# Performance work log

Measured on AMD Instinct MI355X. Metric: run time of the kernel, lower is better.

Reference implementation:

```python
import jax, jax.numpy as jnp
import numpy as np

D_MODEL = 1024
D_QK = 1024
NUM_HEADS = 16
HEAD_DIM = D_QK // NUM_HEADS      # 64
V_DIM = D_MODEL // NUM_HEADS      # 64
B, S = 2, 2048


def setup_inputs() -> dict:
    key = jax.random.key(0)
    ks = jax.random.split(key, 9)
    sc = 0.02
    return {
        "x": jax.random.normal(ks[0], (B, S, D_MODEL), dtype=jnp.float32),
        "Wqk": jax.random.normal(ks[1], (D_MODEL, 2 * D_QK), dtype=jnp.float32) * sc,
        "bqk": jax.random.normal(ks[2], (2 * D_QK,), dtype=jnp.float32) * sc,
        "Wv": jax.random.normal(ks[3], (D_MODEL, D_MODEL), dtype=jnp.float32) * sc,
        "bv": jax.random.normal(ks[4], (D_MODEL,), dtype=jnp.float32) * sc,
        "Wn": jax.random.normal(ks[5], (D_MODEL, NUM_HEADS), dtype=jnp.float32) * sc,
        "bn": jax.random.normal(ks[6], (NUM_HEADS,), dtype=jnp.float32) * sc,
        "Wo": jax.random.normal(ks[7], (D_MODEL, D_MODEL), dtype=jnp.float32) * sc,
        "bo": jax.random.normal(ks[8], (D_MODEL,), dtype=jnp.float32) * sc,
    }


def reference(x, Wqk, bqk, Wv, bv, Wn, bn, Wo, bo):
    b, s, _ = x.shape
    qk = x @ Wqk + bqk                                  # (B,S,2*D_QK)
    v = x @ Wv + bv                                     # (B,S,D_MODEL)
    n = x @ Wn + bn                                     # (B,S,H)

    qk = qk.reshape(b, s, 2, NUM_HEADS, HEAD_DIM)
    q, k = qk[:, :, 0], qk[:, :, 1]                     # (B,S,H,Dh)
    v = v.reshape(b, s, NUM_HEADS, V_DIM)               # (B,S,H,Dv)

    scores = jnp.einsum('bthd,bshd->bhts', q, k)        # (B,H,S,S)
    mask = jnp.tril(jnp.ones((s, s), dtype=scores.dtype))
    n_exp = jnp.exp(jnp.transpose(n, (0, 2, 1)))        # (B,H,S)
    attn = scores * mask / n_exp[:, :, :, None]         # dropout p=0 (eval)

    ctx = jnp.einsum('bhts,bshd->bthd', attn, v)        # (B,S,H,Dv)
    ctx = ctx.reshape(b, s, D_MODEL)
    return ctx @ Wo + bo
```

## Files before the change

### kernel.cpp

```cpp
#include <hip/hip_runtime.h>
#include <hip/hip_bf16.h>

constexpr int Bb   = 2;
constexpr int Ss   = 2048;
constexpr int Dm   = 1024;
constexpr int Hh   = 16;
constexpr int Hd   = 64;
constexpr int Mtot = Bb * Ss;
constexpr int NCH  = Ss / 64;

typedef __bf16 bf16x8 __attribute__((ext_vector_type(8)));
typedef float  f32x4  __attribute__((ext_vector_type(4)));
typedef __attribute__((address_space(1))) unsigned int u32_as1;
typedef __attribute__((address_space(3))) unsigned int u32_as3;

__device__ __forceinline__ void gload_lds16(const void* g, void* l) {
  __builtin_amdgcn_global_load_lds((const u32_as1*)g, (u32_as3*)l, 16, 0, 0);
}

__device__ __forceinline__ unsigned short f2bf(float f) {
  union { float f; unsigned u; } x; x.f = f;
  unsigned r = x.u + 0x7fffu + ((x.u >> 16) & 1u);
  return (unsigned short)(r >> 16);
}

__device__ __forceinline__ float bf2f(unsigned short s) {
  union { unsigned u; float f; } x; x.u = ((unsigned)s) << 16;
  return x.f;
}

__global__ __launch_bounds__(256) void k_prep(
    const float* __restrict__ x, const float* __restrict__ Wn, const float* __restrict__ bn,
    float* __restrict__ invn, unsigned short* __restrict__ xb,
    const float* __restrict__ Wqk, const float* __restrict__ Wv, const float* __restrict__ Wo,
    unsigned short* __restrict__ wprojT, unsigned short* __restrict__ woT) {
  __shared__ __align__(16) char smem[16384];
  int bi = blockIdx.x;
  int tid = threadIdx.x;
  if (bi < 1024) {
    float (*xl)[1024] = (float(*)[1024])smem;
    int w = tid >> 6, lane = tid & 63;
    int row = bi * 4 + w;
    const float4* x4 = (const float4*)(x + (size_t)row * Dm);
    ushort4* xb4 = (ushort4*)(xb + (size_t)row * Dm);
#pragma unroll
    for (int j = 0; j < 4; ++j) {
      float4 v = x4[j * 64 + lane];
      *(float4*)&xl[w][(j * 64 + lane) * 4] = v;
      ushort4 o;
      o.x = f2bf(v.x); o.y = f2bf(v.y); o.z = f2bf(v.z); o.w = f2bf(v.w);
      xb4[j * 64 + lane] = o;
    }
    __syncthreads();
    const float4* Wn4 = (const float4*)Wn;
    f32x4 sum = {0.f, 0.f, 0.f, 0.f};
#pragma unroll 4
    for (int j = 0; j < 64; ++j) {
      float xv = xl[w][j * 16 + (lane >> 2)];
      float4 wv = Wn4[j * 64 + lane];
      sum[0] += xv * wv.x; sum[1] += xv * wv.y; sum[2] += xv * wv.z; sum[3] += xv * wv.w;
    }
#pragma unroll
    for (int m = 4; m < 64; m <<= 1) {
      sum[0] += __shfl_xor(sum[0], m);
      sum[1] += __shfl_xor(sum[1], m);
      sum[2] += __shfl_xor(sum[2], m);
      sum[3] += __shfl_xor(sum[3], m);
    }
    if (lane < 4) {
      int b = row >> 11, s = row & 2047;
#pragma unroll
      for (int e = 0; e < 4; ++e) {
        int h = lane * 4 + e;
        float nv = sum[e] + bn[h];
        invn[((size_t)(b * Hh + h)) * Ss + s] = expf(-nv);
      }
    }
  } else {
    float (*t)[33] = (float(*)[33])smem;
    int ti = bi - 1024;
    const float* W; unsigned short* Wt; int N, n0, k0;
    if (ti < 2048) {
      W = Wqk; Wt = wprojT; N = 2048;
      n0 = (ti & 63) * 32; k0 = (ti >> 6) * 32;
    } else if (ti < 3072) {
      int l = ti - 2048; W = Wv; Wt = wprojT + (size_t)2048 * 1024; N = 1024;
      n0 = (l & 31) * 32; k0 = (l >> 5) * 32;
    } else {
      int l = ti - 3072; W = Wo; Wt = woT; N = 1024;
      n0 = (l & 31) * 32; k0 = (l >> 5) * 32;
    }
    int tx = tid & 31, ty = tid >> 5;
#pragma unroll
    for (int j = 0; j < 32; j += 8)
      t[ty + j][tx] = W[(size_t)(k0 + ty + j) * N + n0 + tx];
    __syncthreads();
#pragma unroll
    for (int j = 0; j < 32; j += 8)
      Wt[(size_t)(n0 + ty + j) * 1024 + k0 + tx] = f2bf(t[tx][ty + j]);
  }
}

__global__ __launch_bounds__(256, 4) void k_gemm_proj(
    const unsigned short* __restrict__ A, const unsigned short* __restrict__ BT,
    const float* __restrict__ bias0, const float* __restrict__ bias1,
    void* __restrict__ out0, void* __restrict__ out1, void* __restrict__ out2,
    void* __restrict__ out3, int M, int N, int K) {
  __shared__ __align__(16) unsigned short SMEM[2 * 128 * 64];
  unsigned short* As = SMEM;
  unsigned short* Bs = SMEM + 128 * 64;
  int tid = threadIdx.x, w = tid >> 6, lane = tid & 63;
  int bid = blockIdx.y * gridDim.x + blockIdx.x;
  int xcd = bid & 7, idx = bid >> 3;
  int m0 = (xcd * 4 + (idx & 3)) * 128;
  int n0 = (idx >> 2) * 128;
  int wm = w >> 1, wn = w & 1;
  f32x4 acc[4][4] = {};

  int csrc = 8 * ((lane & 7) ^ (lane >> 3));
  int rst  = w * 8 + (lane >> 3);
  int rxor = (lane & 7) << 3;

  for (int kt = 0; kt < (K >> 6); ++kt) {
#pragma unroll
    for (int i = 0; i < 4; ++i) {
      int r = i * 32 + rst;
      gload_lds16(A + (size_t)(m0 + r) * K + kt * 64 + csrc, As + i * 2048 + w * 512);
    }
#pragma unroll
    for (int i = 0; i < 4; ++i) {
      int r = i * 32 + rst;
      gload_lds16(BT + (size_t)(n0 + r) * K + kt * 64 + csrc, Bs + i * 2048 + w * 512);
    }
    __syncthreads();
#pragma unroll
    for (int ks = 0; ks < 2; ++ks) {
      int foff = (ks * 32 + (lane >> 4) * 8) ^ rxor;
      bf16x8 af[4], bfr[4];
#pragma unroll
      for (int mt = 0; mt < 4; ++mt)
        af[mt] = *(const bf16x8*)(As + (wm * 64 + mt * 16 + (lane & 15)) * 64 + foff);
#pragma unroll
      for (int nt = 0; nt < 4; ++nt)
        bfr[nt] = *(const bf16x8*)(Bs + (wn * 64 + nt * 16 + (lane & 15)) * 64 + foff);
#pragma unroll
      for (int mt = 0; mt < 4; ++mt)
#pragma unroll
        for (int nt = 0; nt < 4; ++nt)
          acc[mt][nt] = __builtin_amdgcn_mfma_f32_16x16x32_bf16(af[mt], bfr[nt], acc[mt][nt], 0, 0, 0);
    }
    __syncthreads();
  }

  int nfirst = n0 + wn * 64;
  int region = nfirst >> 10;
  unsigned short* eplds = SMEM + w * 4096;

#pragma unroll
  for (int mt = 0; mt < 4; ++mt) {
#pragma unroll
    for (int nt = 0; nt < 4; ++nt) {
      int n = nfirst + nt * 16 + (lane & 15);
      int tbase = m0 + wm * 64 + mt * 16 + (lane >> 4) * 4;
      float bb = (region < 2) ? bias0[n] : bias1[n - 2048];
      if (region <= 1) {
#pragma unroll
        for (int r = 0; r < 4; ++r) {
          int tl = mt * 16 + (lane >> 4) * 4 + r;
          int col = nt * 16 + (lane & 15);
          eplds[tl * 64 + (col ^ ((tl & 7) << 3))] = f2bf(acc[mt][nt][r] + bb);
        }
        if (region == 1) {
          int h = (n >> 6) & 15, d = n & 63, b = tbase >> 11, t = tbase & 2047;
          ushort4 o;
          o.x = f2bf(acc[mt][nt][0] + bb);
          o.y = f2bf(acc[mt][nt][1] + bb);
          o.z = f2bf(acc[mt][nt][2] + bb);
          o.w = f2bf(acc[mt][nt][3] + bb);
          *(ushort4*)((unsigned short*)out2 + ((size_t)(b * Hh + h) * Hd + d) * Ss + t) = o;
        }
      } else {
        int h = (n >> 6) & 15, d = n & 63, b = tbase >> 11, t = tbase & 2047;
        ushort4 o;
        o.x = f2bf(acc[mt][nt][0] + bb);
        o.y = f2bf(acc[mt][nt][1] + bb);
        o.z = f2bf(acc[mt][nt][2] + bb);
        o.w = f2bf(acc[mt][nt][3] + bb);
        *(ushort4*)((unsigned short*)out3 + ((size_t)(b * Hh + h) * Hd + d) * Ss + t) = o;
      }
    }
  }
  if (region <= 1) {
    asm volatile("" ::: "memory");
    int tl = lane;
    int tt = m0 + wm * 64 + tl;
    int b = tt >> 11, t = tt & 2047;
    int h = (nfirst >> 6) & 15;
    unsigned short* dst = ((region == 0) ? (unsigned short*)out0 : (unsigned short*)out1)
                        + (((size_t)(b * Hh + h)) * Ss + t) * Hd;
#pragma unroll
    for (int c = 0; c < 8; ++c) {
      int col = (c * 8) ^ ((tl & 7) << 3);
      *(float4*)(dst + c * 8) = *(const float4*)(eplds + tl * 64 + col);
    }
  }
}

__global__ __launch_bounds__(256, 3) void k_gemm_o(
    const unsigned short* __restrict__ A, const unsigned short* __restrict__ BT,
    const float* __restrict__ bias, float* __restrict__ out) {
  constexpr int K = 1024, N = 1024;
  __shared__ __align__(16) unsigned short As[2][64 * 64];
  __shared__ __align__(16) unsigned short Bs[2][128 * 64];
  int tid = threadIdx.x, w = tid >> 6, lane = tid & 63;
  int bid = blockIdx.y * gridDim.x + blockIdx.x;
  int xcd = bid & 7, idx = bid >> 3;
  int m0 = (xcd * 8 + (idx & 7)) * 64;
  int n0 = (idx >> 3) * 128;
  int wm = w >> 1, wn = w & 1;
  f32x4 acc[2][4] = {};

  int csrc = 8 * ((lane & 7) ^ (lane >> 3));
  int rst  = w * 8 + (lane >> 3);
  int rxor = (lane & 7) << 3;

  auto STAGE = [&](int kt, int cur) {
#pragma unroll
    for (int i = 0; i < 2; ++i) {
      int r = i * 32 + rst;
      gload_lds16(A + (size_t)(m0 + r) * K + kt * 64 + csrc, As[cur] + i * 2048 + w * 512);
    }
#pragma unroll
    for (int i = 0; i < 4; ++i) {
      int r = i * 32 + rst;
      gload_lds16(BT + (size_t)(n0 + r) * K + kt * 64 + csrc, Bs[cur] + i * 2048 + w * 512);
    }
  };

  constexpr int NT = K >> 6;
  STAGE(0, 0);
  __syncthreads();
  for (int kt = 0; kt < NT; ++kt) {
    int cur = kt & 1;
    if (kt + 1 < NT) STAGE(kt + 1, cur ^ 1);
#pragma unroll
    for (int ks = 0; ks < 2; ++ks) {
      int foff = (ks * 32 + (lane >> 4) * 8) ^ rxor;
      bf16x8 af[2], bfr[4];
#pragma unroll
      for (int mt = 0; mt < 2; ++mt)
        af[mt] = *(const bf16x8*)(As[cur] + (wm * 32 + mt * 16 + (lane & 15)) * 64 + foff);
#pragma unroll
      for (int nt = 0; nt < 4; ++nt)
        bfr[nt] = *(const bf16x8*)(Bs[cur] + (wn * 64 + nt * 16 + (lane & 15)) * 64 + foff);
#pragma unroll
      for (int mt = 0; mt < 2; ++mt)
#pragma unroll
        for (int nt = 0; nt < 4; ++nt)
          acc[mt][nt] = __builtin_amdgcn_mfma_f32_16x16x32_bf16(af[mt], bfr[nt], acc[mt][nt], 0, 0, 0);
    }
    __syncthreads();
  }

#pragma unroll
  for (int mt = 0; mt < 2; ++mt) {
#pragma unroll
    for (int nt = 0; nt < 4; ++nt) {
      int n = n0 + wn * 64 + nt * 16 + (lane & 15);
      int m = m0 + wm * 32 + mt * 16 + (lane >> 4) * 4;
      float bb = bias[n];
#pragma unroll
      for (int r = 0; r < 4; ++r)
        out[(size_t)(m + r) * N + n] = acc[mt][nt][r] + bb;
    }
  }
}

__global__ __launch_bounds__(64) void k_gram(
    const unsigned short* __restrict__ vT, const unsigned short* __restrict__ kT,
    unsigned short* __restrict__ G) {
  int lane = threadIdx.x;
  int j = blockIdx.x, bh = blockIdx.y;
  int t0 = j * 64;
  const unsigned short* vb = vT + (size_t)bh * Hd * Ss;
  const unsigned short* kb = kT + (size_t)bh * Hd * Ss;
  unsigned short* g = G + ((size_t)bh * NCH + j) * 4096;

  bf16x8 af[4][2], bfr[4][2];
#pragma unroll
  for (int mt = 0; mt < 4; ++mt)
#pragma unroll
    for (int ks = 0; ks < 2; ++ks) {
      af[mt][ks]  = *(const bf16x8*)(vb + (size_t)(mt * 16 + (lane & 15)) * Ss + t0 + ks * 32 + (lane >> 4) * 8);
      bfr[mt][ks] = *(const bf16x8*)(kb + (size_t)(mt * 16 + (lane & 15)) * Ss + t0 + ks * 32 + (lane >> 4) * 8);
    }
  f32x4 acc[4][4] = {};
#pragma unroll
  for (int mt = 0; mt < 4; ++mt)
#pragma unroll
    for (int nt = 0; nt < 4; ++nt)
#pragma unroll
      for (int ks = 0; ks < 2; ++ks)
        acc[mt][nt] = __builtin_amdgcn_mfma_f32_16x16x32_bf16(af[mt][ks], bfr[nt][ks], acc[mt][nt], 0, 0, 0);
#pragma unroll
  for (int mt = 0; mt < 4; ++mt)
#pragma unroll
    for (int nt = 0; nt < 4; ++nt)
#pragma unroll
      for (int r = 0; r < 4; ++r)
        g[(mt * 16 + (lane >> 4) * 4 + r) * 64 + nt * 16 + (lane & 15)] = f2bf(acc[mt][nt][r]);
}

__global__ __launch_bounds__(256) void k_prefix(
    const unsigned short* __restrict__ G, unsigned short* __restrict__ Sp) {
  int gidx = blockIdx.x * 256 + threadIdx.x;
  int bh = gidx >> 12, e = gidx & 4095;
  const unsigned short* gp = G + (size_t)bh * NCH * 4096 + e;
  unsigned short* sp = Sp + (size_t)bh * NCH * 4096 + e;
  float acc = 0.f;
#pragma unroll
  for (int j = 0; j < NCH; ++j) {
    sp[(size_t)j * 4096] = f2bf(acc);
    acc += bf2f(gp[(size_t)j * 4096]);
  }
}

__global__ __launch_bounds__(256, 6) void k_chunk_attn(
    const unsigned short* __restrict__ q, const unsigned short* __restrict__ k,
    const unsigned short* __restrict__ vT, const unsigned short* __restrict__ Sp,
    const float* __restrict__ invn, unsigned short* __restrict__ ctx) {
  __shared__ __align__(16) unsigned short P[4 * 16 * 64];
  int tid = threadIdx.x, w = tid >> 6, lane = tid & 63;
  int j = blockIdx.x, bh = blockIdx.y;
  int t0 = j * 64;
  const unsigned short* qb = q + (size_t)bh * Ss * Hd;
  const unsigned short* kb = k + (size_t)bh * Ss * Hd;
  const unsigned short* vb = vT + (size_t)bh * Hd * Ss;
  const unsigned short* sp = Sp + ((size_t)bh * NCH + j) * 4096;

  bf16x8 qf[2];
#pragma unroll
  for (int ks = 0; ks < 2; ++ks)
    qf[ks] = *(const bf16x8*)(qb + (size_t)(t0 + w * 16 + (lane & 15)) * Hd + ks * 32 + (lane >> 4) * 8);

  f32x4 acc[4] = {};
#pragma unroll
  for (int nt = 0; nt < 4; ++nt)
#pragma unroll
    for (int ks = 0; ks < 2; ++ks) {
      bf16x8 sf = *(const bf16x8*)(sp + (nt * 16 + (lane & 15)) * 64 + ks * 32 + (lane >> 4) * 8);
      acc[nt] = __builtin_amdgcn_mfma_f32_16x16x32_bf16(qf[ks], sf, acc[nt], 0, 0, 0);
    }

  f32x4 sacc[4] = {};
#pragma unroll
  for (int nt = 0; nt < 4; ++nt)
#pragma unroll
    for (int ks = 0; ks < 2; ++ks) {
      bf16x8 kf = *(const bf16x8*)(kb + (size_t)(t0 + nt * 16 + (lane & 15)) * Hd + ks * 32 + (lane >> 4) * 8);
      sacc[nt] = __builtin_amdgcn_mfma_f32_16x16x32_bf16(qf[ks], kf, sacc[nt], 0, 0, 0);
    }

#pragma unroll
  for (int nt = 0; nt < 4; ++nt)
#pragma unroll
    for (int r = 0; r < 4; ++r) {
      int row = (lane >> 4) * 4 + r;
      int s_local = nt * 16 + (lane & 15);
      float vv = (s_local <= w * 16 + row) ? sacc[nt][r] : 0.f;
      int cb = s_local * 2;
      int byte = w * 2048 + row * 128 + (cb ^ ((row & 7) << 4));
      *(unsigned short*)((char*)P + byte) = f2bf(vv);
    }
  asm volatile("" ::: "memory");

  bf16x8 pf[2];
#pragma unroll
  for (int ks = 0; ks < 2; ++ks) {
    int prow = lane & 15;
    int pcb = (ks * 32 + (lane >> 4) * 8) * 2;
    pf[ks] = *(const bf16x8*)((char*)P + w * 2048 + prow * 128 + (pcb ^ ((prow & 7) << 4)));
  }
#pragma unroll
  for (int dt = 0; dt < 4; ++dt)
#pragma unroll
    for (int ks = 0; ks < 2; ++ks) {
      bf16x8 vf = *(const bf16x8*)(vb + (size_t)(dt * 16 + (lane & 15)) * Ss + t0 + ks * 32 + (lane >> 4) * 8);
      acc[dt] = __builtin_amdgcn_mfma_f32_16x16x32_bf16(pf[ks], vf, acc[dt], 0, 0, 0);
    }

  int b = bh >> 4, h = bh & 15;
  float sc[4];
#pragma unroll
  for (int r = 0; r < 4; ++r)
    sc[r] = invn[(size_t)bh * Ss + t0 + w * 16 + (lane >> 4) * 4 + r];
#pragma unroll
  for (int dt = 0; dt < 4; ++dt)
#pragma unroll
    for (int r = 0; r < 4; ++r) {
      int t = t0 + w * 16 + (lane >> 4) * 4 + r;
      size_t m = (size_t)b * Ss + t;
      ctx[m * Dm + h * Hd + dt * 16 + (lane & 15)] = f2bf(acc[dt][r] * sc[r]);
    }
}

extern "C" void kernel_launch(void* const* d_in, const int* in_sizes, int n_in,
                              void* d_out, int out_size, void* d_ws, size_t ws_size,
                              hipStream_t stream) {
  const float* x   = (const float*)d_in[0];
  const float* Wqk = (const float*)d_in[1];
  const float* bqk = (const float*)d_in[2];
  const float* Wv  = (const float*)d_in[3];
  const float* bv  = (const float*)d_in[4];
  const float* Wn  = (const float*)d_in[5];
  const float* bn  = (const float*)d_in[6];
  const float* Wo  = (const float*)d_in[7];
  const float* bo  = (const float*)d_in[8];

  char* ws = (char*)d_ws;
  size_t off = 0;
  unsigned short* xb    = (unsigned short*)(ws + off); off += (size_t)Mtot * Dm * 2;
  unsigned short* wprojT= (unsigned short*)(ws + off); off += (size_t)3072 * 1024 * 2;
  unsigned short* woT   = (unsigned short*)(ws + off); off += (size_t)1024 * 1024 * 2;
  unsigned short* qbuf  = (unsigned short*)(ws + off); off += (size_t)Bb * Hh * Ss * Hd * 2;
  unsigned short* kbuf  = (unsigned short*)(ws + off); off += (size_t)Bb * Hh * Ss * Hd * 2;
  unsigned short* ktbuf = (unsigned short*)(ws + off); off += (size_t)Bb * Hh * Ss * Hd * 2;
  unsigned short* vbuf  = (unsigned short*)(ws + off); off += (size_t)Bb * Hh * Ss * Hd * 2;
  float* invn           = (float*)(ws + off);          off += (size_t)Bb * Hh * Ss * 4;
  unsigned short* G     = (unsigned short*)(ws + off); off += (size_t)Bb * Hh * NCH * 4096 * 2;
  unsigned short* Sp    = (unsigned short*)(ws + off); off += (size_t)Bb * Hh * NCH * 4096 * 2;
  unsigned short* ctx   = xb;

  k_prep<<<5120, 256, 0, stream>>>(x, Wn, bn, invn, xb, Wqk, Wv, Wo, wprojT, woT);

  k_gemm_proj<<<dim3(3072 / 128, Mtot / 128), 256, 0, stream>>>(
      xb, wprojT, bqk, bv, qbuf, kbuf, ktbuf, vbuf, Mtot, 3072, 1024);

  k_gram<<<dim3(NCH, Bb * Hh), 64, 0, stream>>>(vbuf, ktbuf, G);
  k_prefix<<<(Bb * Hh * 4096) / 256, 256, 0, stream>>>(G, Sp);
  k_chunk_attn<<<dim3(NCH, Bb * Hh), 256, 0, stream>>>(qbuf, kbuf, vbuf, Sp, invn, ctx);

  k_gemm_o<<<dim3(1024 / 128, Mtot / 64), 256, 0, stream>>>(ctx, woT, bo, (float*)d_out);
}
```

Baseline: 101.0 us.

## Triple-buffer projection GEMM K-loop with async LDS prefetch two stages ahead

The projection GEMM main loop changes from a single-buffered K=64 step with two full barriers per step to a three-stage ring of K=32 tiles. Tile t+2 is fetched with direct global-to-LDS loads while tile t feeds the MFMAs, and partial vmcnt waits plus one barrier per step are used. This aims to hide global load latency behind compute and cut synchronisation. In exchange, LDS use grows by half, occupancy drops from 4 to 3 blocks, each step does half the MFMA work, and NT is hardcoded to 32 (so K must be 1024).

```diff
diff --git a/kernel.cpp b/kernel.cpp
--- a/kernel.cpp
+++ b/kernel.cpp
@@ -101,14 +101,12 @@
   }
 }
 
-__global__ __launch_bounds__(256, 4) void k_gemm_proj(
+__global__ __launch_bounds__(256, 3) void k_gemm_proj(
     const unsigned short* __restrict__ A, const unsigned short* __restrict__ BT,
     const float* __restrict__ bias0, const float* __restrict__ bias1,
     void* __restrict__ out0, void* __restrict__ out1, void* __restrict__ out2,
     void* __restrict__ out3, int M, int N, int K) {
-  __shared__ __align__(16) unsigned short SMEM[2 * 128 * 64];
-  unsigned short* As = SMEM;
-  unsigned short* Bs = SMEM + 128 * 64;
+  __shared__ __align__(16) unsigned short SMEM[3 * 128 * 64];
   int tid = threadIdx.x, w = tid >> 6, lane = tid & 63;
   int bid = blockIdx.y * gridDim.x + blockIdx.x;
   int xcd = bid & 7, idx = bid >> 3;
@@ -117,39 +115,49 @@
   int wm = w >> 1, wn = w & 1;
   f32x4 acc[4][4] = {};
 
-  int csrc = 8 * ((lane & 7) ^ (lane >> 3));
-  int rst  = w * 8 + (lane >> 3);
-  int rxor = (lane & 7) << 3;
-
-  for (int kt = 0; kt < (K >> 6); ++kt) {
-#pragma unroll
-    for (int i = 0; i < 4; ++i) {
-      int r = i * 32 + rst;
-      gload_lds16(A + (size_t)(m0 + r) * K + kt * 64 + csrc, As + i * 2048 + w * 512);
-    }
-#pragma unroll
-    for (int i = 0; i < 4; ++i) {
-      int r = i * 32 + rst;
-      gload_lds16(BT + (size_t)(n0 + r) * K + kt * 64 + csrc, Bs + i * 2048 + w * 512);
-    }
-    __syncthreads();
-#pragma unroll
-    for (int ks = 0; ks < 2; ++ks) {
-      int foff = (ks * 32 + (lane >> 4) * 8) ^ rxor;
-      bf16x8 af[4], bfr[4];
-#pragma unroll
-      for (int mt = 0; mt < 4; ++mt)
-        af[mt] = *(const bf16x8*)(As + (wm * 64 + mt * 16 + (lane & 15)) * 64 + foff);
+  int csrc = 8 * ((lane & 3) ^ ((lane >> 2) & 3));
+  int rst  = w * 16 + (lane >> 2);
+  int slotb = (((lane >> 4) ^ (lane & 3)) << 4);
+
+  auto STAGE = [&](int kt, int buf) {
+    unsigned short* base = SMEM + buf * 8192;
+#pragma unroll
+    for (int i = 0; i < 2; ++i) {
+      int r = i * 64 + rst;
+      gload_lds16(A  + (size_t)(m0 + r) * K + kt * 32 + csrc, base + i * 2048 + w * 512);
+      gload_lds16(BT + (size_t)(n0 + r) * K + kt * 32 + csrc, base + 4096 + i * 2048 + w * 512);
+    }
+  };
+
+  STAGE(0, 0);
+  STAGE(1, 1);
+  asm volatile("s_waitcnt vmcnt(4)" ::: "memory");
+  __builtin_amdgcn_s_barrier();
+  asm volatile("" ::: "memory");
+
+  constexpr int NT = 32;
+  for (int t = 0; t < NT; ++t) {
+    int buf = t % 3;
+    const char* Ab = (const char*)(SMEM + buf * 8192);
+    const char* Bv = Ab + 8192;
+    bf16x8 af[4], bfr[4];
+#pragma unroll
+    for (int mt = 0; mt < 4; ++mt)
+      af[mt] = *(const bf16x8*)(Ab + (wm * 64 + mt * 16 + (lane & 15)) * 64 + slotb);
+#pragma unroll
+    for (int nt = 0; nt < 4; ++nt)
+      bfr[nt] = *(const bf16x8*)(Bv + (wn * 64 + nt * 16 + (lane & 15)) * 64 + slotb);
+    if (t + 2 < NT) STAGE(t + 2, (t + 2) % 3);
+#pragma unroll
+    for (int mt = 0; mt < 4; ++mt)
 #pragma unroll
       for (int nt = 0; nt < 4; ++nt)
-        bfr[nt] = *(const bf16x8*)(Bs + (wn * 64 + nt * 16 + (lane & 15)) * 64 + foff);
-#pragma unroll
-      for (int mt = 0; mt < 4; ++mt)
-#pragma unroll
-        for (int nt = 0; nt < 4; ++nt)
-          acc[mt][nt] = __builtin_amdgcn_mfma_f32_16x16x32_bf16(af[mt], bfr[nt], acc[mt][nt], 0, 0, 0);
-    }
-    __syncthreads();
+        acc[mt][nt] = __builtin_amdgcn_mfma_f32_16x16x32_bf16(af[mt], bfr[nt], acc[mt][nt], 0, 0, 0);
+    asm volatile("" ::: "memory");
+    if (t < NT - 2) asm volatile("s_waitcnt vmcnt(4)" ::: "memory");
+    else            asm volatile("s_waitcnt vmcnt(0)" ::: "memory");
+    __builtin_amdgcn_s_barrier();
+    asm volatile("" ::: "memory");
   }
 
   int nfirst = n0 + wn * 64;
```

After: 102.6 us. Within noise of the previous version (+1.6%).
